# Kernel optimization log

Measured on AMD Instinct MI355X. Metric: run time of the kernel, lower is better.

Reference implementation:

```python
import jax, jax.numpy as jnp
import numpy as np

N_NODES = 50000


def _graphconv(h, W, b, src, dst, norm_src, norm_dst, activation):
    # DGL GraphConv, norm='both': scale by out-degree^{-1/2} on src side,
    # aggregate (copy_u + sum), scale by in-degree^{-1/2} on dst side.
    in_f, out_f = W.shape
    h = h * norm_src[:, None]
    if in_f > out_f:
        # mult W first to reduce message size (matches DGL branch)
        h = h @ W
        h = jax.ops.segment_sum(h[src], dst, num_segments=N_NODES)
    else:
        h = jax.ops.segment_sum(h[src], dst, num_segments=N_NODES)
        h = h @ W
    h = h * norm_dst[:, None] + b
    if activation:
        h = jax.nn.relu(h)
    return h


def setup_inputs() -> dict:
    key = jax.random.key(0)
    ks = jax.random.split(key, 10)
    N, E = N_NODES, 800000
    in_feats, n_hidden, n_classes = 256, 128, 64
    features = jax.random.normal(ks[0], (N, in_feats), dtype=jnp.float32)
    src = jax.random.randint(ks[1], (E,), 0, N, dtype=jnp.int32)
    dst = jax.random.randint(ks[2], (E,), 0, N, dtype=jnp.int32)
    def glorot(k, shape):
        lim = float(np.sqrt(6.0 / (shape[0] + shape[1])))
        return jax.random.uniform(k, shape, jnp.float32, -lim, lim)
    return {
        "features": features,
        "W1": glorot(ks[3], (in_feats, n_hidden)), "b1": jnp.zeros((n_hidden,), jnp.float32),
        "W2": glorot(ks[4], (n_hidden, n_hidden)), "b2": jnp.zeros((n_hidden,), jnp.float32),
        "W3": glorot(ks[5], (n_hidden, n_classes)), "b3": jnp.zeros((n_classes,), jnp.float32),
        "src": src, "dst": dst,
    }


def reference(features, W1, b1, W2, b2, W3, b3, src, dst):
    ones = jnp.ones(src.shape, jnp.float32)
    deg_out = jax.ops.segment_sum(ones, src, num_segments=N_NODES)
    deg_in = jax.ops.segment_sum(ones, dst, num_segments=N_NODES)
    norm_src = jax.lax.rsqrt(jnp.maximum(deg_out, 1.0))
    norm_dst = jax.lax.rsqrt(jnp.maximum(deg_in, 1.0))
    h = features
    # dropout in eval mode (identity) for deterministic baseline
    h = _graphconv(h, W1, b1, src, dst, norm_src, norm_dst, activation=True)
    h = _graphconv(h, W2, b2, src, dst, norm_src, norm_dst, activation=True)
    h = _graphconv(h, W3, b3, src, dst, norm_src, norm_dst, activation=False)
    return h
```

## Files before the change

kernel.cpp:

```cpp
#include <hip/hip_runtime.h>
#include <math.h>


typedef _Float16 half8 __attribute__((ext_vector_type(8)));
typedef float floatx4 __attribute__((ext_vector_type(4)));

#define TILE  1024
#define BCAP  8192
#define PKW   64
#define EPT   4
#define SPLIT 4

__global__ __launch_bounds__(256) void bin_edges(
    const int* __restrict__ src, const int* __restrict__ dst, int E, int NB,
    int* __restrict__ gcurD, int* __restrict__ gcurS,
    ushort2* __restrict__ binD, unsigned short* __restrict__ binS)
{
    __shared__ int lcntD[256], curD[256];
    __shared__ int lcntS[256], curS[256];

    const int tid = threadIdx.x;
    const int tile0 = blockIdx.x * TILE;
    const int tn = min(TILE, E - tile0);

    lcntD[tid] = 0;
    lcntS[tid] = 0;
    __syncthreads();

    unsigned short es[EPT], ed[EPT];
    unsigned char ebD[EPT], ebS[EPT];
    int nl = 0;
    for (int i = tid; i < tn; i += 256) {
        int s = src[tile0 + i], d = dst[tile0 + i];
        es[nl] = (unsigned short)s; ed[nl] = (unsigned short)d;
        ebD[nl] = (unsigned char)(d >> 8);
        ebS[nl] = (unsigned char)(s >> 8);
        nl++;
        atomicAdd(&lcntD[d >> 8], 1);
        atomicAdd(&lcntS[s >> 8], 1);
    }
    __syncthreads();

    if (tid < NB) {
        curD[tid] = (lcntD[tid] > 0) ? atomicAdd(&gcurD[tid], lcntD[tid]) : 0;
        curS[tid] = (lcntS[tid] > 0) ? atomicAdd(&gcurS[tid], lcntS[tid]) : 0;
    }
    __syncthreads();

    for (int j = 0; j < nl; j++) {
        int bD = ebD[j];
        int pD = atomicAdd(&curD[bD], 1);
        if (pD < BCAP) {
            ushort2 u; u.x = es[j]; u.y = ed[j];
            binD[(size_t)bD * BCAP + pD] = u;
        }
        int bS = ebS[j];
        int pS = atomicAdd(&curS[bS], 1);
        if (pS < BCAP) binS[(size_t)bS * BCAP + pS] = es[j];
    }
}

__global__ __launch_bounds__(256) void lists_counts(
    const ushort2* __restrict__ binD, const int* __restrict__ gcurD,
    const unsigned short* __restrict__ binS, const int* __restrict__ gcurS,
    unsigned short* __restrict__ packed, int* __restrict__ cntI,
    int* __restrict__ cntO, int N, unsigned short padv)
{
    __shared__ unsigned short stage[64 * PKW];
    __shared__ int lcnt[64];
    __shared__ int h[64];
    const int tid = threadIdx.x;
    const int b = blockIdx.x / SPLIT;
    const int part = blockIdx.x - b * SPLIT;
    const int nlo = (b << 8) + part * 64;

    if (tid < 64) { lcnt[tid] = 0; h[tid] = 0; }
    {
        unsigned int pp = (unsigned int)padv | ((unsigned int)padv << 16);
        uint4 v; v.x = pp; v.y = pp; v.z = pp; v.w = pp;
        for (int i = tid; i < 64 * PKW / 8; i += 256)
            ((uint4*)stage)[i] = v;
    }
    __syncthreads();

    const int nD = min(gcurD[b], BCAP);
    const ushort2* ebD = binD + (size_t)b * BCAP;
    for (int i = tid; i < nD; i += 256) {
        ushort2 e = ebD[i];
        int ld = (int)e.y - nlo;
        if ((unsigned)ld < 64u) {
            int p = atomicAdd(&lcnt[ld], 1);
            if (p < PKW) stage[ld * PKW + p] = e.x;
        }
    }
    const int nS = min(gcurS[b], BCAP);
    const unsigned short* ebS = binS + (size_t)b * BCAP;
    for (int i = tid; i < nS; i += 256) {
        int ls = (int)ebS[i] - nlo;
        if ((unsigned)ls < 64u) atomicAdd(&h[ls], 1);
    }
    __syncthreads();

    if (tid < 64) {
        int node = nlo + tid;
        if (node < N) {
            cntI[node] = min(lcnt[tid], PKW);
            cntO[node] = h[tid];
        }
    }
    const int wave = tid >> 6, lane = tid & 63;
    for (int ld = wave; ld < 64; ld += 4) {
        int nd = nlo + ld;
        if (nd < N)
            packed[(size_t)nd * PKW + lane] = stage[ld * PKW + lane];
    }
}

__global__ __launch_bounds__(256) void wprep(
    const float* __restrict__ W1, const float* __restrict__ W2,
    const float* __restrict__ W3, _Float16* __restrict__ WT1,
    _Float16* __restrict__ WT2, _Float16* __restrict__ WT3,
    int* __restrict__ gcur, _Float16* __restrict__ z0,
    _Float16* __restrict__ z1)
{
    int i = blockIdx.x * 256 + threadIdx.x;
    if (i < 512) gcur[i] = 0;
    else if (i < 640) z0[i - 512] = (_Float16)0.f;
    else if (i < 768) z1[i - 640] = (_Float16)0.f;
    if (i < 256 * 128) {
        int k = i / 128, n = i - k * 128;
        WT1[(size_t)n * 256 + k] = (_Float16)W1[i];
    } else if (i < 256 * 128 + 128 * 128) {
        int r = i - 256 * 128;
        int k = r / 128, n = r - k * 128;
        WT2[(size_t)n * 128 + k] = (_Float16)W2[r];
    } else if (i < 256 * 128 + 128 * 128 + 128 * 64) {
        int r = i - 256 * 128 - 128 * 128;
        int k = r / 64, n = r - k * 64;
        WT3[(size_t)n * 128 + k] = (_Float16)W3[r];
    }
}

template<int K, int NC, bool A_FP32>
__global__ __launch_bounds__(256) void gemm_mfma(
    const void* __restrict__ A_, const _Float16* __restrict__ WT,
    const int* __restrict__ cnt_rs,
    const int* __restrict__ cnt_nd, const float* __restrict__ bias,
    int do_relu, const int* __restrict__ cnt_ns,
    _Float16* __restrict__ C, int M)
{
    constexpr int NT  = NC / 16;
    constexpr int KC  = 128;
    constexpr int LDW = KC + 8;
    __shared__ _Float16 Bs[NC * LDW];

    const int tid  = threadIdx.x;
    const int wave = tid >> 6;
    const int lane = tid & 63;
    const int quad = lane >> 4;
    const int l16  = lane & 15;

    const int row_base = blockIdx.x * 128 + wave * 32;
    const int ar0 = min(row_base + l16, M - 1);
    const int ar1 = min(row_base + 16 + l16, M - 1);

    floatx4 acc[2][NT];
#pragma unroll
    for (int m = 0; m < 2; m++)
#pragma unroll
        for (int t = 0; t < NT; t++)
            acc[m][t] = (floatx4){0.f, 0.f, 0.f, 0.f};

    float rs0 = 1.0f, rs1 = 1.0f;
    if (A_FP32 && cnt_rs) {
        rs0 = rsqrtf(fmaxf((float)cnt_rs[ar0], 1.0f));
        rs1 = rsqrtf(fmaxf((float)cnt_rs[ar1], 1.0f));
    }

    const float*    Af = (const float*)A_;
    const _Float16* Ah = (const _Float16*)A_;

    for (int kc = 0; kc < K; kc += KC) {
#pragma unroll
        for (int s = tid; s < NC * (KC / 8); s += 256) {
            int row  = s >> 4;
            int col8 = s & 15;
            half8 v = *(const half8*)&WT[(size_t)row * K + kc + col8 * 8];
            *(half8*)&Bs[row * LDW + col8 * 8] = v;
        }
        __syncthreads();
#pragma unroll
        for (int k0 = 0; k0 < KC; k0 += 32) {
            half8 a0, a1;
            if (A_FP32) {
                const float* p0 = &Af[(size_t)ar0 * K + kc + k0 + quad * 8];
                const float* p1 = &Af[(size_t)ar1 * K + kc + k0 + quad * 8];
                float4 f0 = *(const float4*)p0;
                float4 f1 = *(const float4*)(p0 + 4);
                float4 g0 = *(const float4*)p1;
                float4 g1 = *(const float4*)(p1 + 4);
                a0[0] = (_Float16)(f0.x * rs0); a0[1] = (_Float16)(f0.y * rs0);
                a0[2] = (_Float16)(f0.z * rs0); a0[3] = (_Float16)(f0.w * rs0);
                a0[4] = (_Float16)(f1.x * rs0); a0[5] = (_Float16)(f1.y * rs0);
                a0[6] = (_Float16)(f1.z * rs0); a0[7] = (_Float16)(f1.w * rs0);
                a1[0] = (_Float16)(g0.x * rs1); a1[1] = (_Float16)(g0.y * rs1);
                a1[2] = (_Float16)(g0.z * rs1); a1[3] = (_Float16)(g0.w * rs1);
                a1[4] = (_Float16)(g1.x * rs1); a1[5] = (_Float16)(g1.y * rs1);
                a1[6] = (_Float16)(g1.z * rs1); a1[7] = (_Float16)(g1.w * rs1);
            } else {
                a0 = *(const half8*)&Ah[(size_t)ar0 * K + kc + k0 + quad * 8];
                a1 = *(const half8*)&Ah[(size_t)ar1 * K + kc + k0 + quad * 8];
            }
#pragma unroll
            for (int t = 0; t < NT; t++) {
                half8 b = *(const half8*)&Bs[(t * 16 + l16) * LDW + k0 + quad * 8];
                acc[0][t] = __builtin_amdgcn_mfma_f32_16x16x32_f16(a0, b, acc[0][t], 0, 0, 0);
                acc[1][t] = __builtin_amdgcn_mfma_f32_16x16x32_f16(a1, b, acc[1][t], 0, 0, 0);
            }
        }
        __syncthreads();
    }

#pragma unroll
    for (int m = 0; m < 2; m++) {
#pragma unroll
        for (int t = 0; t < NT; t++) {
            int col = t * 16 + l16;
            float bv = bias ? bias[col] : 0.f;
#pragma unroll
            for (int r = 0; r < 4; r++) {
                int row_o = row_base + m * 16 + quad * 4 + r;
                if (row_o < M) {
                    float v = acc[m][t][r];
                    if (cnt_nd) v *= rsqrtf(fmaxf((float)cnt_nd[row_o], 1.0f));
                    v += bv;
                    if (do_relu) v = fmaxf(v, 0.f);
                    if (cnt_ns) v *= rsqrtf(fmaxf((float)cnt_ns[row_o], 1.0f));
                    C[(size_t)row_o * NC + col] = (_Float16)v;
                }
            }
        }
    }
}

__global__ __launch_bounds__(512) void layer23(
    const _Float16* __restrict__ H1s, const int* __restrict__ cntI,
    const int* __restrict__ cntO, const unsigned short* __restrict__ packed,
    const _Float16* __restrict__ WT2, const _Float16* __restrict__ WT3,
    const float* __restrict__ b2, _Float16* __restrict__ M3, int N)
{
    constexpr int LDW = 136;
    __shared__ _Float16 agg[128 * LDW];
    __shared__ _Float16 Bs[128 * LDW];

    const int tid  = threadIdx.x;
    const int w    = tid >> 6;
    const int lane = tid & 63;
    const int quad = lane >> 4;
    const int l16  = lane & 15;
    const int grp  = lane >> 4;
    const int base = blockIdx.x * 128;

    if (blockIdx.x == 0 && tid < 8) {
        half8 zv;
#pragma unroll
        for (int h = 0; h < 8; h++) zv[h] = (_Float16)0.f;
        ((half8*)(M3 + (size_t)N * 64))[tid] = zv;
    }

    const half8* mp = (const half8*)H1s;
    for (int i = 0; i < 16; i++) {
        const int row  = w * 16 + i;
        const int node = base + row;
        float a[8];
#pragma unroll
        for (int h = 0; h < 8; h++) a[h] = 0.f;
        if (node < N) {
            int len = cntI[node];
            const unsigned short* bl = packed + (size_t)node * PKW;
            int iters = (len + 15) >> 4;
            if (iters < 1) iters = 1;
            for (int it = 0; it < iters; it++) {
                int j = it * 16 + grp;
                int s0 = bl[j], s1 = bl[j + 4], s2 = bl[j + 8], s3 = bl[j + 12];
                half8 v0 = mp[(size_t)s0 * 16 + l16];
                half8 v1 = mp[(size_t)s1 * 16 + l16];
                half8 v2 = mp[(size_t)s2 * 16 + l16];
                half8 v3 = mp[(size_t)s3 * 16 + l16];
#pragma unroll
                for (int h = 0; h < 8; h++)
                    a[h] += ((float)v0[h] + (float)v1[h]) + ((float)v2[h] + (float)v3[h]);
            }
#pragma unroll
            for (int h = 0; h < 8; h++) {
                a[h] += __shfl_xor(a[h], 16);
                a[h] += __shfl_xor(a[h], 32);
            }
        }
        if (grp == 0) {
            half8 rv;
#pragma unroll
            for (int h = 0; h < 8; h++) rv[h] = (_Float16)a[h];
            *(half8*)&agg[row * LDW + l16 * 8] = rv;
        }
    }
    __syncthreads();

#pragma unroll
    for (int s = tid; s < 128 * 16; s += 512) {
        int row = s >> 4, col8 = s & 15;
        *(half8*)&Bs[row * LDW + col8 * 8] =
            *(const half8*)&WT2[(size_t)row * 128 + col8 * 8];
    }
    __syncthreads();

    floatx4 acc[8];
#pragma unroll
    for (int t = 0; t < 8; t++) acc[t] = (floatx4){0.f, 0.f, 0.f, 0.f};
#pragma unroll
    for (int k0 = 0; k0 < 128; k0 += 32) {
        half8 a0 = *(const half8*)&agg[(w * 16 + l16) * LDW + k0 + quad * 8];
#pragma unroll
        for (int t = 0; t < 8; t++) {
            half8 b = *(const half8*)&Bs[(t * 16 + l16) * LDW + k0 + quad * 8];
            acc[t] = __builtin_amdgcn_mfma_f32_16x16x32_f16(a0, b, acc[t], 0, 0, 0);
        }
    }
    float rsI_[4], rsO_[4];
#pragma unroll
    for (int r = 0; r < 4; r++) {
        int row_o = base + w * 16 + quad * 4 + r;
        int ro = min(row_o, N - 1);
        rsI_[r] = rsqrtf(fmaxf((float)cntI[ro], 1.0f));
        rsO_[r] = rsqrtf(fmaxf((float)cntO[ro], 1.0f));
    }
#pragma unroll
    for (int t = 0; t < 8; t++) {
        int col = t * 16 + l16;
        float bv = b2[col];
#pragma unroll
        for (int r = 0; r < 4; r++) {
            int row_l = w * 16 + quad * 4 + r;
            float v = acc[t][r] * rsI_[r] + bv;
            v = fmaxf(v, 0.f);
            v *= rsO_[r];
            agg[row_l * LDW + col] = (_Float16)v;
        }
    }
    __syncthreads();

#pragma unroll
    for (int s = tid; s < 64 * 16; s += 512) {
        int row = s >> 4, col8 = s & 15;
        *(half8*)&Bs[row * LDW + col8 * 8] =
            *(const half8*)&WT3[(size_t)row * 128 + col8 * 8];
    }
    __syncthreads();

    floatx4 acc3[4];
#pragma unroll
    for (int t = 0; t < 4; t++) acc3[t] = (floatx4){0.f, 0.f, 0.f, 0.f};
#pragma unroll
    for (int k0 = 0; k0 < 128; k0 += 32) {
        half8 a0 = *(const half8*)&agg[(w * 16 + l16) * LDW + k0 + quad * 8];
#pragma unroll
        for (int t = 0; t < 4; t++) {
            half8 b = *(const half8*)&Bs[(t * 16 + l16) * LDW + k0 + quad * 8];
            acc3[t] = __builtin_amdgcn_mfma_f32_16x16x32_f16(a0, b, acc3[t], 0, 0, 0);
        }
    }
#pragma unroll
    for (int t = 0; t < 4; t++) {
        int col = t * 16 + l16;
#pragma unroll
        for (int r = 0; r < 4; r++) {
            int row_o = base + w * 16 + quad * 4 + r;
            if (row_o < N)
                M3[(size_t)row_o * 64 + col] = (_Float16)acc3[t][r];
        }
    }
}

__global__ __launch_bounds__(256) void gather128(
    const _Float16* __restrict__ msg, const int* __restrict__ cntI,
    const int* __restrict__ cntO, const unsigned short* __restrict__ packed,
    const float* __restrict__ bias, int do_relu, int use_nd, int use_ns,
    _Float16* __restrict__ out, int N)
{
    int node = (blockIdx.x * 256 + threadIdx.x) >> 6;
    if (node >= N) return;
    int lane = threadIdx.x & 63;
    int grp = lane >> 4, l16 = lane & 15;

    int len = min(cntI[node], PKW);
    const unsigned short* bl = packed + (size_t)node * PKW;
    const half8* mp = (const half8*)msg;

    float a[8];
#pragma unroll
    for (int h = 0; h < 8; h++) a[h] = 0.f;

    int iters = (len + 15) >> 4;
    if (iters < 1) iters = 1;
    for (int it = 0; it < iters; it++) {
        int j = it * 16 + grp;
        int s0 = bl[j], s1 = bl[j + 4], s2 = bl[j + 8], s3 = bl[j + 12];
        half8 v0 = mp[(size_t)s0 * 16 + l16];
        half8 v1 = mp[(size_t)s1 * 16 + l16];
        half8 v2 = mp[(size_t)s2 * 16 + l16];
        half8 v3 = mp[(size_t)s3 * 16 + l16];
#pragma unroll
        for (int h = 0; h < 8; h++)
            a[h] += ((float)v0[h] + (float)v1[h]) + ((float)v2[h] + (float)v3[h]);
    }
#pragma unroll
    for (int h = 0; h < 8; h++) {
        a[h] += __shfl_xor(a[h], 16);
        a[h] += __shfl_xor(a[h], 32);
    }

    if (grp == 0) {
        float sc = use_nd ? rsqrtf(fmaxf((float)len, 1.0f)) : 1.0f;
        float pp = use_ns ? rsqrtf(fmaxf((float)cntO[node], 1.0f)) : 1.0f;
        half8 rv;
#pragma unroll
        for (int h = 0; h < 8; h++) {
            float bv = bias ? bias[l16 * 8 + h] : 0.f;
            float r = a[h] * sc + bv;
            if (do_relu) r = fmaxf(r, 0.f);
            rv[h] = (_Float16)(r * pp);
        }
        ((half8*)out)[(size_t)node * 16 + l16] = rv;
    }
}

__global__ __launch_bounds__(256) void gather64(
    const _Float16* __restrict__ msg, const int* __restrict__ cntI,
    const unsigned short* __restrict__ packed, const float* __restrict__ bias,
    float* __restrict__ out, int N)
{
    int node = (blockIdx.x * 256 + threadIdx.x) >> 6;
    if (node >= N) return;
    int lane = threadIdx.x & 63;
    int grp = lane >> 3, l8 = lane & 7;

    int len = min(cntI[node], PKW);
    const unsigned short* bl = packed + (size_t)node * PKW;
    const half8* mp = (const half8*)msg;

    float a[8];
#pragma unroll
    for (int h = 0; h < 8; h++) a[h] = 0.f;

    int iters = (len + 15) >> 4;
    if (iters < 1) iters = 1;
    for (int it = 0; it < iters; it++) {
        int j = it * 16 + grp;
        int s0 = bl[j], s1 = bl[j + 8];
        half8 v0 = mp[(size_t)s0 * 8 + l8];
        half8 v1 = mp[(size_t)s1 * 8 + l8];
#pragma unroll
        for (int h = 0; h < 8; h++)
            a[h] += (float)v0[h] + (float)v1[h];
    }
#pragma unroll
    for (int h = 0; h < 8; h++) {
        a[h] += __shfl_xor(a[h], 8);
        a[h] += __shfl_xor(a[h], 16);
        a[h] += __shfl_xor(a[h], 32);
    }

    if (grp == 0) {
        float sc = rsqrtf(fmaxf((float)len, 1.0f));
        float4 r0, r1;
        r0.x = a[0] * sc + bias[l8 * 8 + 0];
        r0.y = a[1] * sc + bias[l8 * 8 + 1];
        r0.z = a[2] * sc + bias[l8 * 8 + 2];
        r0.w = a[3] * sc + bias[l8 * 8 + 3];
        r1.x = a[4] * sc + bias[l8 * 8 + 4];
        r1.y = a[5] * sc + bias[l8 * 8 + 5];
        r1.z = a[6] * sc + bias[l8 * 8 + 6];
        r1.w = a[7] * sc + bias[l8 * 8 + 7];
        float4* op = (float4*)&out[(size_t)node * 64 + l8 * 8];
        op[0] = r0;
        op[1] = r1;
    }
}

extern "C" void kernel_launch(void* const* d_in, const int* in_sizes, int n_in,
                              void* d_out, int out_size, void* d_ws, size_t ws_size,
                              hipStream_t stream)
{
    const float* X  = (const float*)d_in[0];
    const float* W1 = (const float*)d_in[1];
    const float* b1 = (const float*)d_in[2];
    const float* W2 = (const float*)d_in[3];
    const float* b2 = (const float*)d_in[4];
    const float* W3 = (const float*)d_in[5];
    const float* b3 = (const float*)d_in[6];
    const int*   src = (const int*)d_in[7];
    const int*   dst = (const int*)d_in[8];

    const int N = in_sizes[0] / 256;
    const int E = in_sizes[7];
    const int NB = (N + 255) >> 8;

    char* base = (char*)d_ws;
    size_t cur = 0;
    auto alloc = [&](size_t bytes) -> void* {
        void* p = base + cur;
        cur += (bytes + 255) & ~(size_t)255;
        return p;
    };
    int* gcur2 = (int*)alloc((size_t)2 * 256 * 4);
    int* gcurD = gcur2;
    int* gcurS = gcur2 + 256;
    ushort2*        binD   = (ushort2*)alloc((size_t)NB * BCAP * 4);
    unsigned short* binS   = (unsigned short*)alloc((size_t)NB * BCAP * 2);
    unsigned short* packed = (unsigned short*)alloc((size_t)N * PKW * 2);
    int* cntO = (int*)alloc((size_t)N * 4);
    int* cntI = (int*)alloc((size_t)N * 4);
    _Float16* Bh0 = (_Float16*)alloc(((size_t)N + 1) * 128 * 2);
    _Float16* Bh1 = (_Float16*)alloc(((size_t)N + 1) * 128 * 2);
    _Float16* WT1 = (_Float16*)alloc((size_t)256 * 128 * 2);
    _Float16* WT2 = (_Float16*)alloc((size_t)128 * 128 * 2);
    _Float16* WT3 = (_Float16*)alloc((size_t)128 * 64 * 2);

    const int tblk = (E + TILE - 1) / TILE;
    const int gblk = (N + 127) / 128;
    const int wblk = (N + 3) / 4;

    wprep<<<(256*128 + 128*128 + 128*64 + 255) / 256, 256, 0, stream>>>(
        W1, W2, W3, WT1, WT2, WT3,
        gcur2, Bh0 + (size_t)N * 128, Bh1 + (size_t)N * 128);
    bin_edges<<<tblk, 256, 0, stream>>>(src, dst, E, NB, gcurD, gcurS, binD, binS);
    lists_counts<<<NB * SPLIT, 256, 0, stream>>>(binD, gcurD, binS, gcurS,
                                                 packed, cntI, cntO, N,
                                                 (unsigned short)N);

    gemm_mfma<256, 128, true><<<gblk, 256, 0, stream>>>(
        X, WT1, cntO, nullptr, nullptr, 0, nullptr, Bh0, N);
    gather128<<<wblk, 256, 0, stream>>>(
        Bh0, cntI, cntO, packed, b1, 1, 1, 1, Bh1, N);

    layer23<<<gblk, 512, 0, stream>>>(
        Bh1, cntI, cntO, packed, WT2, WT3, b2, Bh0, N);

    gather64<<<wblk, 256, 0, stream>>>(
        Bh0, cntI, packed, b3, (float*)d_out, N);
}
```

Measured before the change: 269.0 us.

## Halve layer23 tile to 64 rows and read weights directly from global

```diff
diff --git a/kernel.cpp b/kernel.cpp
--- a/kernel.cpp
+++ b/kernel.cpp
@@ -250,16 +250,14 @@
     const float* __restrict__ b2, _Float16* __restrict__ M3, int N)
 {
     constexpr int LDW = 136;
-    __shared__ _Float16 agg[128 * LDW];
-    __shared__ _Float16 Bs[128 * LDW];
+    __shared__ _Float16 agg[64 * LDW];
 
     const int tid  = threadIdx.x;
     const int w    = tid >> 6;
     const int lane = tid & 63;
     const int quad = lane >> 4;
     const int l16  = lane & 15;
-    const int grp  = lane >> 4;
-    const int base = blockIdx.x * 128;
+    const int base = blockIdx.x * 64;
 
     if (blockIdx.x == 0 && tid < 8) {
         half8 zv;
@@ -269,8 +267,8 @@
     }
 
     const half8* mp = (const half8*)H1s;
-    for (int i = 0; i < 16; i++) {
-        const int row  = w * 16 + i;
+    for (int i = 0; i < 8; i++) {
+        const int row  = w * 8 + i;
         const int node = base + row;
         float a[8];
 #pragma unroll
@@ -281,7 +279,7 @@
             int iters = (len + 15) >> 4;
             if (iters < 1) iters = 1;
             for (int it = 0; it < iters; it++) {
-                int j = it * 16 + grp;
+                int j = it * 16 + quad;
                 int s0 = bl[j], s1 = bl[j + 4], s2 = bl[j + 8], s3 = bl[j + 12];
                 half8 v0 = mp[(size_t)s0 * 16 + l16];
                 half8 v1 = mp[(size_t)s1 * 16 + l16];
@@ -297,7 +295,7 @@
                 a[h] += __shfl_xor(a[h], 32);
             }
         }
-        if (grp == 0) {
+        if (quad == 0) {
             half8 rv;
 #pragma unroll
             for (int h = 0; h < 8; h++) rv[h] = (_Float16)a[h];
@@ -306,42 +304,44 @@
     }
     __syncthreads();
 
-#pragma unroll
-    for (int s = tid; s < 128 * 16; s += 512) {
-        int row = s >> 4, col8 = s & 15;
-        *(half8*)&Bs[row * LDW + col8 * 8] =
-            *(const half8*)&WT2[(size_t)row * 128 + col8 * 8];
-    }
-    __syncthreads();
-
-    floatx4 acc[8];
-#pragma unroll
-    for (int t = 0; t < 8; t++) acc[t] = (floatx4){0.f, 0.f, 0.f, 0.f};
-#pragma unroll
-    for (int k0 = 0; k0 < 128; k0 += 32) {
-        half8 a0 = *(const half8*)&agg[(w * 16 + l16) * LDW + k0 + quad * 8];
-#pragma unroll
-        for (int t = 0; t < 8; t++) {
-            half8 b = *(const half8*)&Bs[(t * 16 + l16) * LDW + k0 + quad * 8];
-            acc[t] = __builtin_amdgcn_mfma_f32_16x16x32_f16(a0, b, acc[t], 0, 0, 0);
-        }
-    }
+    const int mw = w & 3, half = w >> 2;
+
+    half8 a0[4];
+#pragma unroll
+    for (int kk = 0; kk < 4; kk++)
+        a0[kk] = *(const half8*)&agg[(mw * 16 + l16) * LDW + kk * 32 + quad * 8];
+
+    floatx4 acc[4];
+#pragma unroll
+    for (int tt = 0; tt < 4; tt++) acc[tt] = (floatx4){0.f, 0.f, 0.f, 0.f};
+#pragma unroll
+    for (int tt = 0; tt < 4; tt++) {
+        int t = half * 4 + tt;
+#pragma unroll
+        for (int kk = 0; kk < 4; kk++) {
+            half8 b = *(const half8*)&WT2[(size_t)(t * 16 + l16) * 128 + kk * 32 + quad * 8];
+            acc[tt] = __builtin_amdgcn_mfma_f32_16x16x32_f16(a0[kk], b, acc[tt], 0, 0, 0);
+        }
+    }
+
+    __syncthreads();
+
     float rsI_[4], rsO_[4];
 #pragma unroll
     for (int r = 0; r < 4; r++) {
-        int row_o = base + w * 16 + quad * 4 + r;
+        int row_o = base + mw * 16 + quad * 4 + r;
         int ro = min(row_o, N - 1);
         rsI_[r] = rsqrtf(fmaxf((float)cntI[ro], 1.0f));
         rsO_[r] = rsqrtf(fmaxf((float)cntO[ro], 1.0f));
     }
 #pragma unroll
-    for (int t = 0; t < 8; t++) {
-        int col = t * 16 + l16;
+    for (int tt = 0; tt < 4; tt++) {
+        int col = (half * 4 + tt) * 16 + l16;
         float bv = b2[col];
 #pragma unroll
         for (int r = 0; r < 4; r++) {
-            int row_l = w * 16 + quad * 4 + r;
-            float v = acc[t][r] * rsI_[r] + bv;
+            int row_l = mw * 16 + quad * 4 + r;
+            float v = acc[tt][r] * rsI_[r] + bv;
             v = fmaxf(v, 0.f);
             v *= rsO_[r];
             agg[row_l * LDW + col] = (_Float16)v;
@@ -349,34 +349,31 @@
     }
     __syncthreads();
 
-#pragma unroll
-    for (int s = tid; s < 64 * 16; s += 512) {
-        int row = s >> 4, col8 = s & 15;
-        *(half8*)&Bs[row * LDW + col8 * 8] =
-            *(const half8*)&WT3[(size_t)row * 128 + col8 * 8];
-    }
-    __syncthreads();
-
-    floatx4 acc3[4];
-#pragma unroll
-    for (int t = 0; t < 4; t++) acc3[t] = (floatx4){0.f, 0.f, 0.f, 0.f};
-#pragma unroll
-    for (int k0 = 0; k0 < 128; k0 += 32) {
-        half8 a0 = *(const half8*)&agg[(w * 16 + l16) * LDW + k0 + quad * 8];
-#pragma unroll
-        for (int t = 0; t < 4; t++) {
-            half8 b = *(const half8*)&Bs[(t * 16 + l16) * LDW + k0 + quad * 8];
-            acc3[t] = __builtin_amdgcn_mfma_f32_16x16x32_f16(a0, b, acc3[t], 0, 0, 0);
-        }
-    }
-#pragma unroll
-    for (int t = 0; t < 4; t++) {
-        int col = t * 16 + l16;
+    half8 c0[4];
+#pragma unroll
+    for (int kk = 0; kk < 4; kk++)
+        c0[kk] = *(const half8*)&agg[(mw * 16 + l16) * LDW + kk * 32 + quad * 8];
+
+    floatx4 acc3[2];
+#pragma unroll
+    for (int tt = 0; tt < 2; tt++) acc3[tt] = (floatx4){0.f, 0.f, 0.f, 0.f};
+#pragma unroll
+    for (int tt = 0; tt < 2; tt++) {
+        int t = half * 2 + tt;
+#pragma unroll
+        for (int kk = 0; kk < 4; kk++) {
+            half8 b = *(const half8*)&WT3[(size_t)(t * 16 + l16) * 128 + kk * 32 + quad * 8];
+            acc3[tt] = __builtin_amdgcn_mfma_f32_16x16x32_f16(c0[kk], b, acc3[tt], 0, 0, 0);
+        }
+    }
+#pragma unroll
+    for (int tt = 0; tt < 2; tt++) {
+        int col = (half * 2 + tt) * 16 + l16;
 #pragma unroll
         for (int r = 0; r < 4; r++) {
-            int row_o = base + w * 16 + quad * 4 + r;
+            int row_o = base + mw * 16 + quad * 4 + r;
             if (row_o < N)
-                M3[(size_t)row_o * 64 + col] = (_Float16)acc3[t][r];
+                M3[(size_t)row_o * 64 + col] = (_Float16)acc3[tt][r];
         }
     }
 }
@@ -528,6 +525,7 @@
 
     const int tblk = (E + TILE - 1) / TILE;
     const int gblk = (N + 127) / 128;
+    const int lblk = (N + 63) / 64;
     const int wblk = (N + 3) / 4;
 
     wprep<<<(256*128 + 128*128 + 128*64 + 255) / 256, 256, 0, stream>>>(
@@ -543,7 +541,7 @@
     gather128<<<wblk, 256, 0, stream>>>(
         Bh0, cntI, cntO, packed, b1, 1, 1, 1, Bh1, N);
 
-    layer23<<<gblk, 512, 0, stream>>>(
+    layer23<<<lblk, 512, 0, stream>>>(
         Bh1, cntI, cntO, packed, WT2, WT3, b2, Bh0, N);
 
     gather64<<<wblk, 256, 0, stream>>>(
```

New measurement: 283.9 us. 5.5% more time.
